# Kernel tuning notes

Hardware: AMD Instinct MI355X
Metric: run time of the kernel (lower is better)

The kernel has to match this reference:

```python
import jax, jax.numpy as jnp
import numpy as np

G, DIN, DOUT, R = 8, 1024, 1024, 16
N = 8192
SCALE = 32.0 / 16.0  # alpha / r


def grouped_linear(x, W, mask):
    """Grouped linear: out[n] = x[n] @ W[g[n]].
    x: [N, din], W: [G, din, dout], mask: [N, G] one-hot (float).
    Computed as all-group matmul + select; the fused grouped-GEMM is the
    kernel opportunity this reference baselines."""
    y_all = jnp.einsum('ni,gio->gno', x, W)      # [G, N, dout]
    return jnp.einsum('gno,ng->no', y_all, mask)  # [N, dout]


def setup_inputs() -> dict:
    key = jax.random.key(0)
    k1, k2, k3, k4, k5 = jax.random.split(key, 5)
    x = jax.random.normal(k1, (N, DIN), dtype=jnp.float32)
    x_groups = jnp.sort(jax.random.randint(k2, (N,), 0, G, dtype=jnp.int64))
    W_base = jax.random.normal(k3, (G, DIN, DOUT), dtype=jnp.float32) * 0.02
    W_A = jax.random.normal(k4, (G, DIN, R), dtype=jnp.float32) * 0.02
    # original inits lora_B to zero; use small random values so the LoRA path
    # contributes nonzero signal for correctness testing
    W_B = jax.random.normal(k5, (G, R, DOUT), dtype=jnp.float32) * 0.02
    return {"x": x, "x_groups": x_groups, "W_base": W_base, "W_A": W_A, "W_B": W_B}


def reference(x, x_groups, W_base, W_A, W_B):
    mask = (x_groups[:, None] == jnp.arange(G)).astype(x.dtype)  # [N, G] one-hot
    base = grouped_linear(x, W_base, mask)            # base GroupedLinear
    a = grouped_linear(x, W_A, mask)                  # lora_A (dropout p=0 -> identity)
    adapt = grouped_linear(a, W_B, mask)              # lora_B
    return base + SCALE * adapt
```

## Files before the change

### kernel.cpp

```cpp
#include <hip/hip_runtime.h>
#include <stdint.h>

#define N_TOK 8192
#define DIN   1024
#define DOUT  1024
#define NG    8
#define LSCALE 2.0f
#define WROWS (DOUT + 16)

typedef __attribute__((ext_vector_type(4))) float  float4v;
typedef __attribute__((ext_vector_type(8))) short  short8;
typedef short8  frag_ab;
typedef float4v frag_cd;

__device__ __forceinline__ short f2bf(float f) {
    union { float f; uint32_t u; } v; v.f = f;
    uint32_t r = v.u + 0x7fffu + ((v.u >> 16) & 1u);
    return (short)(r >> 16);
}

__device__ __forceinline__ void load_lds16(const void* g, void* lds) {
    __builtin_amdgcn_global_load_lds(
        (const __attribute__((address_space(1))) uint32_t*)g,
        (__attribute__((address_space(3))) uint32_t*)lds,
        16, 0, 0);
}

#define PREP_GRID 6273

__global__ __launch_bounds__(256) void prep_kernel(
        const float* __restrict__ x, const float* __restrict__ Wb,
        const float* __restrict__ WA, const float* __restrict__ WB,
        const int* __restrict__ groups,
        short* __restrict__ xb, short* __restrict__ WtA,
        short* __restrict__ WBt, int* __restrict__ starts) {
    __shared__ float tile[64][65];
    const int blk = blockIdx.x, t = threadIdx.x;

    if (blk < 4096) {
        size_t idx = (size_t)(blk * 256 + t) * 8;
        const float4v* p = (const float4v*)(x + idx);
        float4v a = p[0], b = p[1];
        short8 o;
        o[0]=f2bf(a[0]); o[1]=f2bf(a[1]); o[2]=f2bf(a[2]); o[3]=f2bf(a[3]);
        o[4]=f2bf(b[0]); o[5]=f2bf(b[1]); o[6]=f2bf(b[2]); o[7]=f2bf(b[3]);
        *(short8*)(xb + idx) = o;
    } else if (blk < 6144) {
        int b = blk - 4096;
        int g = b >> 8, rem = b & 255;
        int n0 = (rem & 15) * 64, k0 = (rem >> 4) * 64;
        const float* Wg = Wb + (size_t)g * DIN * DOUT;
#pragma unroll
        for (int i = 0; i < 4; ++i) {
            int idx = i * 256 + t;
            int r = idx >> 4, c = (idx & 15) * 4;
            float4v v = *(const float4v*)(Wg + (size_t)(k0 + r) * DOUT + n0 + c);
            tile[r][c+0]=v[0]; tile[r][c+1]=v[1]; tile[r][c+2]=v[2]; tile[r][c+3]=v[3];
        }
        __syncthreads();
        short* Wtg = WtA + (size_t)g * WROWS * DIN;
#pragma unroll
        for (int i = 0; i < 2; ++i) {
            int idx = i * 256 + t;
            int n = idx >> 3, c8 = (idx & 7) * 8;
            short8 o;
#pragma unroll
            for (int j = 0; j < 8; ++j) o[j] = f2bf(tile[c8 + j][n]);
            *(short8*)(Wtg + (size_t)(n0 + n) * DIN + k0 + c8) = o;
        }
    } else if (blk < 6176) {
        int idx = (blk - 6144) * 256 + t;
        int g = idx >> 10, n = idx & 1023;
        const float* src = WB + (size_t)g * 16 * DOUT + n;
        short8 o0, o1;
#pragma unroll
        for (int r = 0; r < 8; ++r) o0[r] = f2bf(src[(size_t)r * DOUT]);
#pragma unroll
        for (int r = 0; r < 8; ++r) o1[r] = f2bf(src[(size_t)(r + 8) * DOUT]);
        short* dst = WBt + (size_t)idx * 32;
        *(short8*)dst        = o0;
        *(short8*)(dst + 8)  = o1;
        *(short8*)(dst + 16) = (short8)0;
        *(short8*)(dst + 24) = (short8)0;
    } else if (blk < 6240) {
        int tid = (blk - 6176) * 256 + t;
        size_t o = (size_t)tid * 8;
        int g  = (int)(o >> 14);
        int rm = (int)(o & 16383);
        int r  = rm >> 10;
        int k0 = rm & 1023;
        const float* src = WA + (size_t)g * DIN * 16 + r;
        short8 ov;
#pragma unroll
        for (int j = 0; j < 8; ++j) ov[j] = f2bf(src[(size_t)(k0 + j) * 16]);
        *(short8*)(WtA + ((size_t)g * WROWS + DOUT + r) * DIN + k0) = ov;
    } else {
        int i = (blk - 6240) * 256 + t;
        if (i > N_TOK) return;
        int cur  = (i < N_TOK) ? groups[i] : NG;
        int prev = (i == 0) ? -1 : groups[i - 1];
        for (int g = prev + 1; g <= cur; ++g) starts[g] = i;
    }
}

#define BM 128
#define BN 128
#define BK 64
#define BROWS (BN + 16)

__global__ __launch_bounds__(256, 2)
void gemm_grouped(const short* __restrict__ xb,
                  const short* __restrict__ WtA,
                  const short* __restrict__ WBt,
                  const int*   __restrict__ starts,
                  float* __restrict__ out) {
    __shared__ short As[BM * BK];
    __shared__ short Bs[BROWS * BK];

    const int t    = threadIdx.x;
    const int lane = t & 63;
    const int wid  = t >> 6;
    const int L        = blockIdx.x;
    const int row_tile = (L & 7) * 8 + (L >> 6);
    const int col_tile = (L >> 3) & 7;
    const int col0 = col_tile * BN;
    const int row0 = row_tile * BM;
    const int wr   = (wid >> 1) * 64;
    const int wc   = (wid & 1) * 64;
    const int m16  = lane & 15;
    const int q    = lane >> 4;
    const bool do_a = (wid & 1) == 0;

    int gbeg = 0;
    while (starts[gbeg + 1] <= row0) ++gbeg;

    for (int g = gbeg; g < NG && starts[g] < row0 + BM; ++g) {
        const int rlo = starts[g]     > row0      ? starts[g]     : row0;
        const int rhi = starts[g + 1] < row0 + BM ? starts[g + 1] : row0 + BM;
        if (rlo >= rhi) continue;

        const short* wg = WtA + (size_t)g * WROWS * DIN;

        frag_cd acc[4][4];
        frag_cd acc_a[4];
#pragma unroll
        for (int i = 0; i < 4; ++i) {
#pragma unroll
            for (int j = 0; j < 4; ++j) { frag_cd z = {0.f,0.f,0.f,0.f}; acc[i][j] = z; }
            frag_cd z = {0.f,0.f,0.f,0.f}; acc_a[i] = z;
        }

        __syncthreads();

        for (int kt = 0; kt < DIN; kt += BK) {
#pragma unroll
            for (int i = 0; i < 4; ++i) {
                int Lc = i * 256 + t;
                int r  = Lc >> 3;
                int c8 = (Lc & 7) ^ (r & 7);
                load_lds16(xb + (size_t)(row0 + r) * DIN + kt + c8 * 8,
                           &As[(i * 256 + wid * 64) * 8]);
            }
#pragma unroll
            for (int i = 0; i < 4; ++i) {
                int Lc = i * 256 + t;
                int r  = Lc >> 3;
                int c8 = (Lc & 7) ^ (r & 7);
                load_lds16(wg + (size_t)(col0 + r) * DIN + kt + c8 * 8,
                           &Bs[(i * 256 + wid * 64) * 8]);
            }
            if (t < 128) {
                int rr = t >> 3;
                int c8 = (t & 7) ^ (rr & 7);
                load_lds16(wg + ((size_t)DOUT + rr) * DIN + kt + c8 * 8,
                           &Bs[(1024 + wid * 64) * 8]);
            }
            __syncthreads();

#pragma unroll
            for (int kk = 0; kk < BK; kk += 32) {
                frag_ab af[4], bf[4];
                const int ch = (kk >> 3) + q;
#pragma unroll
                for (int mi = 0; mi < 4; ++mi) {
                    int rr = wr + mi * 16 + m16;
                    af[mi] = *(const frag_ab*)&As[rr * BK + ((ch ^ (rr & 7)) << 3)];
                }
#pragma unroll
                for (int ni = 0; ni < 4; ++ni) {
                    int cc = wc + ni * 16 + m16;
                    bf[ni] = *(const frag_ab*)&Bs[cc * BK + ((ch ^ (cc & 7)) << 3)];
                }
#pragma unroll
                for (int mi = 0; mi < 4; ++mi)
#pragma unroll
                    for (int ni = 0; ni < 4; ++ni)
                        acc[mi][ni] = __builtin_amdgcn_mfma_f32_16x16x32_bf16(
                            af[mi], bf[ni], acc[mi][ni], 0, 0, 0);
                if (do_a) {
                    int cc = 128 + m16;
                    frag_ab ba = *(const frag_ab*)&Bs[cc * BK + ((ch ^ (cc & 7)) << 3)];
#pragma unroll
                    for (int mi = 0; mi < 4; ++mi)
                        acc_a[mi] = __builtin_amdgcn_mfma_f32_16x16x32_bf16(
                            af[mi], ba, acc_a[mi], 0, 0, 0);
                }
            }
            __syncthreads();
        }

        short* a_lds = As;
        {
            int row = t >> 1, cz = 16 + (t & 1) * 8;
            *(short8*)&a_lds[row * 40 + cz] = (short8)0;
        }
        if (do_a) {
#pragma unroll
            for (int mi = 0; mi < 4; ++mi)
#pragma unroll
                for (int r = 0; r < 4; ++r) {
                    int row = wr + mi * 16 + q * 4 + r;
                    a_lds[row * 40 + m16] = f2bf(acc_a[mi][r] * LSCALE);
                }
        }
        __syncthreads();
        {
            frag_ab af[4], bfw[4];
#pragma unroll
            for (int mi = 0; mi < 4; ++mi)
                af[mi] = *(const frag_ab*)&a_lds[(wr + mi * 16 + m16) * 40 + q * 8];
#pragma unroll
            for (int ni = 0; ni < 4; ++ni)
                bfw[ni] = *(const frag_ab*)&WBt[((size_t)g * DOUT + col0 + wc + ni * 16 + m16) * 32 + q * 8];
#pragma unroll
            for (int mi = 0; mi < 4; ++mi)
#pragma unroll
                for (int ni = 0; ni < 4; ++ni)
                    acc[mi][ni] = __builtin_amdgcn_mfma_f32_16x16x32_bf16(
                        af[mi], bfw[ni], acc[mi][ni], 0, 0, 0);
        }

#pragma unroll
        for (int mi = 0; mi < 4; ++mi)
#pragma unroll
            for (int r = 0; r < 4; ++r) {
                int grow = row0 + wr + mi * 16 + q * 4 + r;
                if (grow >= rlo && grow < rhi) {
                    float* orow = out + (size_t)grow * DOUT + col0 + wc + m16;
#pragma unroll
                    for (int ni = 0; ni < 4; ++ni) orow[ni * 16] = acc[mi][ni][r];
                }
            }
    }
}

extern "C" void kernel_launch(void* const* d_in, const int* in_sizes, int n_in,
                              void* d_out, int out_size, void* d_ws, size_t ws_size,
                              hipStream_t stream) {
    const float* x      = (const float*)d_in[0];
    const int*   groups = (const int*)d_in[1];
    const float* Wb     = (const float*)d_in[2];
    const float* WA     = (const float*)d_in[3];
    const float* WB     = (const float*)d_in[4];
    float* out = (float*)d_out;

    char* ws = (char*)d_ws;
    int*   starts = (int*)ws;
    short* xb     = (short*)(ws + 1024);
    short* WtA    = (short*)(ws + 1024 + (size_t)16 * 1024 * 1024);
    short* WBt    = (short*)(ws + 1024 + (size_t)33 * 1024 * 1024);

    hipLaunchKernelGGL(prep_kernel, dim3(PREP_GRID), dim3(256), 0, stream,
                       x, Wb, WA, WB, groups, xb, WtA, WBt, starts);
    hipLaunchKernelGGL(gemm_grouped, dim3(512), dim3(256), 0, stream,
                       xb, WtA, WBt, starts, out);
}
```

Measured before the change: 149.5 us.

## Double-buffer LDS tiles and load LoRA-A weights directly from global

Splits the As/Bs shared-memory tiles into two buffers so the next K-slice is prefetched via global_load_lds while MFMAs run on the current one. This drops the mid-iteration barrier, leaving one sync per K step. The 16 LoRA-A weight rows are no longer staged in LDS; the A-computing waves read them straight from global into registers each iteration. LDS use roughly doubles, which may hurt the two-blocks-per-CU occupancy, and the direct global reads of the A weights are uncoalesced.

```diff
diff --git a/kernel.cpp b/kernel.cpp
--- a/kernel.cpp
+++ b/kernel.cpp
@@ -106,7 +106,7 @@
 #define BM 128
 #define BN 128
 #define BK 64
-#define BROWS (BN + 16)
+#define NKT (DIN / BK)
 
 __global__ __launch_bounds__(256, 2)
 void gemm_grouped(const short* __restrict__ xb,
@@ -114,8 +114,8 @@
                   const short* __restrict__ WBt,
                   const int*   __restrict__ starts,
                   float* __restrict__ out) {
-    __shared__ short As[BM * BK];
-    __shared__ short Bs[BROWS * BK];
+    __shared__ short As[2][BM * BK];
+    __shared__ short Bs[2][BN * BK];
 
     const int t    = threadIdx.x;
     const int lane = t & 63;
@@ -152,30 +152,41 @@
 
         __syncthreads();
 
-        for (int kt = 0; kt < DIN; kt += BK) {
-#pragma unroll
-            for (int i = 0; i < 4; ++i) {
-                int Lc = i * 256 + t;
-                int r  = Lc >> 3;
-                int c8 = (Lc & 7) ^ (r & 7);
-                load_lds16(xb + (size_t)(row0 + r) * DIN + kt + c8 * 8,
-                           &As[(i * 256 + wid * 64) * 8]);
+#define STAGE(buf, kt)                                                        \
+        {                                                                     \
+            _Pragma("unroll")                                                 \
+            for (int i = 0; i < 4; ++i) {                                     \
+                int Lc = i * 256 + t;                                         \
+                int r  = Lc >> 3;                                             \
+                int c8 = (Lc & 7) ^ (r & 7);                                  \
+                load_lds16(xb + (size_t)(row0 + r) * DIN + (kt) + c8 * 8,     \
+                           &As[buf][(i * 256 + wid * 64) * 8]);               \
+            }                                                                 \
+            _Pragma("unroll")                                                 \
+            for (int i = 0; i < 4; ++i) {                                     \
+                int Lc = i * 256 + t;                                         \
+                int r  = Lc >> 3;                                             \
+                int c8 = (Lc & 7) ^ (r & 7);                                  \
+                load_lds16(wg + (size_t)(col0 + r) * DIN + (kt) + c8 * 8,     \
+                           &Bs[buf][(i * 256 + wid * 64) * 8]);               \
+            }                                                                 \
+        }
+
+        STAGE(0, 0);
+        __syncthreads();
+
+#pragma unroll 2
+        for (int kt_i = 0; kt_i < NKT; ++kt_i) {
+            const int cur = kt_i & 1;
+            const int kt  = kt_i * BK;
+            if (kt_i + 1 < NKT) STAGE(cur ^ 1, kt + BK);
+
+            frag_ab ba0, ba1;
+            if (do_a) {
+                const short* tp = wg + (size_t)(DOUT + m16) * DIN + kt + q * 8;
+                ba0 = *(const frag_ab*)tp;
+                ba1 = *(const frag_ab*)(tp + 32);
             }
-#pragma unroll
-            for (int i = 0; i < 4; ++i) {
-                int Lc = i * 256 + t;
-                int r  = Lc >> 3;
-                int c8 = (Lc & 7) ^ (r & 7);
-                load_lds16(wg + (size_t)(col0 + r) * DIN + kt + c8 * 8,
-                           &Bs[(i * 256 + wid * 64) * 8]);
-            }
-            if (t < 128) {
-                int rr = t >> 3;
-                int c8 = (t & 7) ^ (rr & 7);
-                load_lds16(wg + ((size_t)DOUT + rr) * DIN + kt + c8 * 8,
-                           &Bs[(1024 + wid * 64) * 8]);
-            }
-            __syncthreads();
 
 #pragma unroll
             for (int kk = 0; kk < BK; kk += 32) {
@@ -184,12 +195,12 @@
 #pragma unroll
                 for (int mi = 0; mi < 4; ++mi) {
                     int rr = wr + mi * 16 + m16;
-                    af[mi] = *(const frag_ab*)&As[rr * BK + ((ch ^ (rr & 7)) << 3)];
+                    af[mi] = *(const frag_ab*)&As[cur][rr * BK + ((ch ^ (rr & 7)) << 3)];
                 }
 #pragma unroll
                 for (int ni = 0; ni < 4; ++ni) {
                     int cc = wc + ni * 16 + m16;
-                    bf[ni] = *(const frag_ab*)&Bs[cc * BK + ((ch ^ (cc & 7)) << 3)];
+                    bf[ni] = *(const frag_ab*)&Bs[cur][cc * BK + ((ch ^ (cc & 7)) << 3)];
                 }
 #pragma unroll
                 for (int mi = 0; mi < 4; ++mi)
@@ -198,8 +209,7 @@
                         acc[mi][ni] = __builtin_amdgcn_mfma_f32_16x16x32_bf16(
                             af[mi], bf[ni], acc[mi][ni], 0, 0, 0);
                 if (do_a) {
-                    int cc = 128 + m16;
-                    frag_ab ba = *(const frag_ab*)&Bs[cc * BK + ((ch ^ (cc & 7)) << 3)];
+                    frag_ab ba = kk ? ba1 : ba0;
 #pragma unroll
                     for (int mi = 0; mi < 4; ++mi)
                         acc_a[mi] = __builtin_amdgcn_mfma_f32_16x16x32_bf16(
@@ -208,8 +218,9 @@
             }
             __syncthreads();
         }
-
-        short* a_lds = As;
+#undef STAGE
+
+        short* a_lds = As[0];
         {
             int row = t >> 1, cz = 16 + (t & 1) * 8;
             *(short8*)&a_lds[row * 40 + cz] = (short8)0;
```

After: 157.9 us. 5.6% more time.
